# Kernel optimization log

Hardware: AMD Instinct MI355X
Metric: run time of the kernel (lower is better)

The kernel has to match this reference:

```python
import jax, jax.numpy as jnp
import numpy as np

THRESHOLD = 0.5
NEG_POS_RATIO = 3
ALPHA = 10.0
N_PRIORS = 8732
N_CLASSES = 21
BATCH = 128
N_OBJ = 32


def cxcy_to_xy(cxcy):
    return jnp.concatenate([cxcy[..., :2] - cxcy[..., 2:] / 2.0,
                            cxcy[..., :2] + cxcy[..., 2:] / 2.0], axis=-1)


def xy_to_cxcy(xy):
    return jnp.concatenate([(xy[..., :2] + xy[..., 2:]) / 2.0,
                            xy[..., 2:] - xy[..., :2]], axis=-1)


def cxcy_to_gcxgcy(cxcy, priors_cxcy):
    return jnp.concatenate([(cxcy[..., :2] - priors_cxcy[..., :2]) / (priors_cxcy[..., 2:] / 10.0),
                            jnp.log(cxcy[..., 2:] / priors_cxcy[..., 2:]) * 5.0], axis=-1)


def find_jaccard_overlap(a, b):
    # a: (M,4) xyxy, b: (P,4) xyxy -> (M,P)
    lt = jnp.maximum(a[:, None, :2], b[None, :, :2])
    rb = jnp.minimum(a[:, None, 2:], b[None, :, 2:])
    wh = jnp.clip(rb - lt, 0.0)
    inter = wh[..., 0] * wh[..., 1]
    area_a = (a[:, 2] - a[:, 0]) * (a[:, 3] - a[:, 1])
    area_b = (b[:, 2] - b[:, 0]) * (b[:, 3] - b[:, 1])
    return inter / (area_a[:, None] + area_b[None, :] - inter)


def _match_one(boxes, labels, priors_xy, priors_cxcy):
    # boxes: (M,4) xyxy, labels: (M,)
    iou = find_jaccard_overlap(boxes, priors_xy)           # (M,P)
    obj_idx = jnp.argmax(iou, axis=1)                      # best prior per object
    iou = iou.at[jnp.arange(boxes.shape[0]), obj_idx].set(1.0)
    positive = (iou >= THRESHOLD).any(axis=0)              # (P,)
    max_prior_idx = jnp.argmax(iou, axis=0)                # best object per prior
    true_cls = labels[max_prior_idx] * positive.astype(labels.dtype)
    matched = boxes[max_prior_idx]                         # (P,4)
    true_locs = cxcy_to_gcxgcy(xy_to_cxcy(matched), priors_cxcy)
    return true_locs, true_cls, positive


def setup_inputs() -> dict:
    key = jax.random.key(0)
    k1, k2, k3, k4, k5, k6 = jax.random.split(key, 6)
    pred_loc = jax.random.normal(k1, (BATCH, N_PRIORS, 4), dtype=jnp.float32)
    pred_cls = jax.random.normal(k2, (BATCH, N_PRIORS, N_CLASSES), dtype=jnp.float32)
    # valid xyxy gt boxes in [0,1]
    p1 = jax.random.uniform(k3, (BATCH, N_OBJ, 2))
    p2 = jax.random.uniform(k4, (BATCH, N_OBJ, 2))
    b_boxes = jnp.concatenate([jnp.minimum(p1, p2), jnp.maximum(p1, p2) + 1e-3], axis=-1)
    b_boxes = jnp.clip(b_boxes, 0.0, 1.0).astype(jnp.float32)
    b_labels = jax.random.randint(k5, (BATCH, N_OBJ), 1, N_CLASSES)
    cxy = jax.random.uniform(k6, (N_PRIORS, 2), minval=0.1, maxval=0.9)
    wh = jax.random.uniform(jax.random.fold_in(k6, 1), (N_PRIORS, 2), minval=0.05, maxval=0.3)
    priors_cxcy = jnp.concatenate([cxy, wh], axis=-1).astype(jnp.float32)
    return {"pred_loc": pred_loc, "pred_cls": pred_cls, "b_boxes": b_boxes,
            "b_labels": b_labels, "priors_cxcy": priors_cxcy}


def reference(pred_loc, pred_cls, b_boxes, b_labels, priors_cxcy):
    batch_size, n_priors, n_classes = pred_cls.shape
    priors_xy = cxcy_to_xy(priors_cxcy)
    true_locs, true_classes, positive = jax.vmap(
        _match_one, in_axes=(0, 0, None, None))(b_boxes, b_labels, priors_xy, priors_cxcy)
    pos_f = positive.astype(pred_loc.dtype)                 # (B,P)
    n_positives = positive.sum(axis=1)                      # (B,)
    n_pos_total = n_positives.sum().astype(pred_loc.dtype)
    # L1 loss (mean over positive box elements)
    loc_loss = (jnp.abs(pred_loc - true_locs) * pos_f[..., None]).sum() / (n_pos_total * 4.0)
    # per-prior cross-entropy
    logp = jax.nn.log_softmax(pred_cls, axis=-1)
    ce = -jnp.take_along_axis(logp, true_classes[..., None], axis=-1)[..., 0]  # (B,P)
    conf_loss_pos = (ce * pos_f).sum()
    # hard negative mining: sort negatives descending per image
    conf_neg = jnp.where(positive, 0.0, ce)
    conf_neg_sorted = -jnp.sort(-conf_neg, axis=1)
    ranks = jnp.arange(n_priors)[None, :]
    hard_mask = ranks < (NEG_POS_RATIO * n_positives)[:, None]
    conf_loss_hard_neg = jnp.where(hard_mask, conf_neg_sorted, 0.0).sum()
    conf_loss = (conf_loss_hard_neg + conf_loss_pos) / n_pos_total
    loc_loss = ALPHA * loc_loss
    total_loss = conf_loss + loc_loss
    return total_loss, loc_loss, conf_loss
```

## Files before the change

kernel.cpp:

```cpp
#include <hip/hip_runtime.h>
#include <math.h>

#define B 128
#define M 32
#define P 8732
#define C 21
#define ALPHA 10.0f
#define TPB2 256
#define PPT 4
#define PPB (TPB2 * PPT)
#define NB2 9

__global__ __launch_bounds__(256) void k1_objargmax(
    const float* __restrict__ b_boxes, const float* __restrict__ priors,
    int* __restrict__ objidx, int* __restrict__ done) {
  if (blockIdx.x == 0 && threadIdx.x == 0) *done = 0;
  int wid = threadIdx.x >> 6;
  int lane = threadIdx.x & 63;
  int task = blockIdx.x * 4 + wid;
  if (task >= B * M) return;
  const float* bx = b_boxes + (size_t)task * 4;
  float x1 = bx[0], y1 = bx[1], x2 = bx[2], y2 = bx[3];
  float areaA = (x2 - x1) * (y2 - y1);
  float best = -1.0f;
  int bi = P;
  for (int p = lane; p < P; p += 64) {
    float4 pr = ((const float4*)priors)[p];
    float pw2 = pr.z * 0.5f, ph2 = pr.w * 0.5f;
    float iw = fminf(x2, pr.x + pw2) - fmaxf(x1, pr.x - pw2);
    float ih = fminf(y2, pr.y + ph2) - fmaxf(y1, pr.y - ph2);
    iw = fmaxf(iw, 0.0f);
    ih = fmaxf(ih, 0.0f);
    float inter = iw * ih;
    float iou = inter / (areaA + pr.z * pr.w - inter);
    if (iou > best) { best = iou; bi = p; }
  }
  for (int off = 32; off >= 1; off >>= 1) {
    float ov = __shfl_xor(best, off, 64);
    int oi = __shfl_xor(bi, off, 64);
    if (ov > best || (ov == best && oi < bi)) { best = ov; bi = oi; }
  }
  if (lane == 0) objidx[task] = bi;
}

__global__ __launch_bounds__(TPB2) void k2_perprior(
    const float* __restrict__ pred_loc, const float* __restrict__ pred_cls,
    const float* __restrict__ b_boxes, const int* __restrict__ b_labels,
    const float* __restrict__ priors, const int* __restrict__ objidx,
    float* __restrict__ ploc, float* __restrict__ pce, int* __restrict__ pnp,
    float* __restrict__ confneg) {
  int b = blockIdx.y;
  int p0 = blockIdx.x * PPB;
  int tid = threadIdx.x;

  __shared__ float sx1[M], sy1[M], sx2[M], sy2[M], sarea[M];
  __shared__ int slab[M], sobj[M];
  if (tid < M) {
    int m = tid;
    float4 bx = ((const float4*)b_boxes)[b * M + m];
    sx1[m] = bx.x; sy1[m] = bx.y; sx2[m] = bx.z; sy2[m] = bx.w;
    sarea[m] = (bx.z - bx.x) * (bx.w - bx.y);
    slab[m] = b_labels[b * M + m];
    sobj[m] = objidx[b * M + m];
  }
  __syncthreads();

  float locpart = 0.0f, cepospart = 0.0f;
  int npos = 0;
  int pbase = p0 + tid * PPT;
  if (pbase < P) {
    float4 pr[PPT], pl[PPT];
    const float4* prp = (const float4*)priors + pbase;
    const float4* plp = (const float4*)pred_loc + (size_t)b * P + pbase;
#pragma unroll
    for (int j = 0; j < PPT; j++) { pr[j] = prp[j]; pl[j] = plp[j]; }

    float px1[PPT], py1[PPT], px2[PPT], py2[PPT], areaP[PPT], best[PPT];
    int bm[PPT];
#pragma unroll
    for (int j = 0; j < PPT; j++) {
      float pw2 = pr[j].z * 0.5f, ph2 = pr[j].w * 0.5f;
      px1[j] = pr[j].x - pw2; py1[j] = pr[j].y - ph2;
      px2[j] = pr[j].x + pw2; py2[j] = pr[j].y + ph2;
      areaP[j] = pr[j].z * pr[j].w;
      best[j] = -1.0f; bm[j] = 0;
    }
    for (int m = 0; m < M; m++) {
      float bx1 = sx1[m], by1 = sy1[m], bx2 = sx2[m], by2 = sy2[m];
      float ar = sarea[m];
      int so = sobj[m];
#pragma unroll
      for (int j = 0; j < PPT; j++) {
        float iw = fminf(bx2, px2[j]) - fmaxf(bx1, px1[j]);
        float ih = fminf(by2, py2[j]) - fmaxf(by1, py1[j]);
        iw = fmaxf(iw, 0.0f);
        ih = fmaxf(ih, 0.0f);
        float inter = iw * ih;
        float iou = inter / (ar + areaP[j] - inter);
        if (so == pbase + j) iou = 1.0f;
        if (iou > best[j]) { best[j] = iou; bm[j] = m; }
      }
    }

    const float4* pc4t =
        (const float4*)(pred_cls + ((size_t)b * P + p0) * C) + 21 * tid;
    float4 cn;
    float* cnp = (float*)&cn;
#pragma unroll
    for (int j = 0; j < PPT; j++) {
      bool pos = best[j] >= 0.5f;
      int mj = bm[j];
      int cls = pos ? slab[mj] : 0;
      float bx1 = sx1[mj], by1 = sy1[mj], bx2 = sx2[mj], by2 = sy2[mj];
      float cx = (bx1 + bx2) * 0.5f, cy = (by1 + by2) * 0.5f;
      float w = bx2 - bx1, h = by2 - by1;
      float g0 = (cx - pr[j].x) * 10.0f / pr[j].z;
      float g1 = (cy - pr[j].y) * 10.0f / pr[j].w;
      float g2 = __logf(w / pr[j].z) * 5.0f;
      float g3 = __logf(h / pr[j].w) * 5.0f;
      if (pos) {
        locpart += fabsf(pl[j].x - g0) + fabsf(pl[j].y - g1) +
                   fabsf(pl[j].z - g2) + fabsf(pl[j].w - g3);
        npos++;
      }
      float4 u4[6];
#pragma unroll
      for (int q = 0; q < 6; q++) u4[q] = pc4t[5 * j + q];
      const float* u = (const float*)u4;
      float mx = u[j];
#pragma unroll
      for (int c = 1; c < C; c++) mx = fmaxf(mx, u[j + c]);
      float se = 0.0f;
      float vc = u[j];
#pragma unroll
      for (int c = 0; c < C; c++) {
        float x = u[j + c];
        se += __expf(x - mx);
        if (c == cls) vc = x;
      }
      float ce = mx + __logf(se) - vc;
      cnp[j] = pos ? 0.0f : ce;
      cepospart += pos ? ce : 0.0f;
    }
    ((float4*)confneg)[((size_t)b * P + pbase) >> 2] = cn;
  }

  for (int off = 32; off >= 1; off >>= 1) {
    locpart += __shfl_down(locpart, off, 64);
    cepospart += __shfl_down(cepospart, off, 64);
    npos += __shfl_down(npos, off, 64);
  }
  __shared__ float rloc[4], rce[4];
  __shared__ int rnp[4];
  int wid = tid >> 6;
  if ((tid & 63) == 0) { rloc[wid] = locpart; rce[wid] = cepospart; rnp[wid] = npos; }
  __syncthreads();
  if (tid == 0) {
    int f = b * NB2 + blockIdx.x;
    ploc[f] = rloc[0] + rloc[1] + rloc[2] + rloc[3];
    pce[f] = rce[0] + rce[1] + rce[2] + rce[3];
    pnp[f] = rnp[0] + rnp[1] + rnp[2] + rnp[3];
  }
}

__global__ __launch_bounds__(1024) void k3_hardneg(
    const float* __restrict__ confneg,
    const float* __restrict__ ploc, const float* __restrict__ pce,
    const int* __restrict__ pnp,
    float* __restrict__ imgres, int* __restrict__ done,
    float* __restrict__ out) {
  int b = blockIdx.x;
  int tid = threadIdx.x;
  int wid = tid >> 6;
  int lane = tid & 63;

  __shared__ float s[P];
  __shared__ int histw[16 * 256];
  __shared__ __align__(16) int cnt[256];
  __shared__ int sdig, scum, sK, sLast;
  __shared__ float sLoc, sCe, sNp;
  __shared__ float rsum[16], rl[16], rc[16], rh[16], rn[16];
  __shared__ int rcnt[16];

  const float* row = confneg + (size_t)b * P;
  for (int i = tid; i < P; i += 1024) s[i] = row[i];

  if (wid == 0) {
    float lp = 0.0f, cp = 0.0f;
    int np = 0;
    if (lane < NB2) {
      int f = b * NB2 + lane;
      lp = ploc[f]; cp = pce[f]; np = pnp[f];
    }
    for (int off = 32; off >= 1; off >>= 1) {
      lp += __shfl_down(lp, off, 64);
      cp += __shfl_down(cp, off, 64);
      np += __shfl_down(np, off, 64);
    }
    if (lane == 0) {
      int K = np * 3;
      if (K > P) K = P;
      sK = K; sLoc = lp; sCe = cp; sNp = (float)np;
    }
  }
  __syncthreads();

  int K = sK;
  unsigned pfx = 0;
  int Krem = K;
#pragma unroll
  for (int pass = 3; pass >= 0; --pass) {
    int sh = pass * 8;
    for (int i = tid; i < 16 * 256; i += 1024) histw[i] = 0;
    __syncthreads();
    unsigned himask = (pass == 3) ? 0u : (0xFFFFFFFFu << (sh + 8));
    int* myh = &histw[wid * 256];
    for (int i = tid; i < P; i += 1024) {
      unsigned ub = __float_as_uint(s[i]);
      if ((ub & himask) == pfx) atomicAdd(&myh[(ub >> sh) & 255], 1);
    }
    __syncthreads();
    if (tid < 256) {
      int c = 0;
#pragma unroll
      for (int w = 0; w < 16; w++) c += histw[w * 256 + tid];
      cnt[tid] = c;
    }
    __syncthreads();
    if (wid == 0) {
      int4 c4 = ((const int4*)cnt)[lane];
      int s3 = c4.w;
      int s2 = c4.z + s3;
      int s1 = c4.y + s2;
      int s0 = c4.x + s1;
      int suf = s0;
      for (int off = 1; off < 64; off <<= 1) {
        int t = __shfl_down(suf, off, 64);
        if (lane + off < 64) suf += t;
      }
      int above = suf - s0;
      int S0 = above + s0, S1 = above + s1, S2 = above + s2, S3 = above + s3;
      int S4 = above;
      if (S3 >= Krem && S4 < Krem) { sdig = 4 * lane + 3; scum = S4; }
      else if (S2 >= Krem && S3 < Krem) { sdig = 4 * lane + 2; scum = S3; }
      else if (S1 >= Krem && S2 < Krem) { sdig = 4 * lane + 1; scum = S2; }
      else if (S0 >= Krem && S1 < Krem) { sdig = 4 * lane + 0; scum = S1; }
    }
    __syncthreads();
    pfx |= ((unsigned)sdig) << sh;
    Krem -= scum;
  }
  float tau = __uint_as_float(pfx);

  float sum = 0.0f;
  int cgt = 0;
  for (int i = tid; i < P; i += 1024) {
    float v = s[i];
    if (v > tau) { sum += v; cgt++; }
  }
  for (int off = 32; off >= 1; off >>= 1) {
    sum += __shfl_down(sum, off, 64);
    cgt += __shfl_down(cgt, off, 64);
  }
  if (lane == 0) { rsum[wid] = sum; rcnt[wid] = cgt; }
  __syncthreads();
  if (tid == 0) {
    float stot = 0.0f;
    int ctot = 0;
#pragma unroll
    for (int w = 0; w < 16; w++) { stot += rsum[w]; ctot += rcnt[w]; }
    float hard = stot + (float)(K - ctot) * tau;
    imgres[b * 4 + 0] = sLoc;
    imgres[b * 4 + 1] = sCe;
    imgres[b * 4 + 2] = hard;
    imgres[b * 4 + 3] = sNp;
    __threadfence();
    int prev = atomicAdd(done, 1);
    sLast = (prev == B - 1) ? 1 : 0;
  }
  __syncthreads();
  if (sLast) {
    __threadfence();
    float l = 0.0f, c = 0.0f, h = 0.0f, n = 0.0f;
    if (tid < B) {
      l = atomicAdd(&imgres[tid * 4 + 0], 0.0f);
      c = atomicAdd(&imgres[tid * 4 + 1], 0.0f);
      h = atomicAdd(&imgres[tid * 4 + 2], 0.0f);
      n = atomicAdd(&imgres[tid * 4 + 3], 0.0f);
    }
    for (int off = 32; off >= 1; off >>= 1) {
      l += __shfl_down(l, off, 64);
      c += __shfl_down(c, off, 64);
      h += __shfl_down(h, off, 64);
      n += __shfl_down(n, off, 64);
    }
    if (lane == 0) { rl[wid] = l; rc[wid] = c; rh[wid] = h; rn[wid] = n; }
    __syncthreads();
    if (tid == 0) {
      float L = 0, Cc = 0, H = 0, N = 0;
#pragma unroll
      for (int w = 0; w < 16; w++) { L += rl[w]; Cc += rc[w]; H += rh[w]; N += rn[w]; }
      float loc = ALPHA * L / (N * 4.0f);
      float conf = (H + Cc) / N;
      out[0] = conf + loc;
      out[1] = loc;
      out[2] = conf;
    }
  }
}

extern "C" void kernel_launch(void* const* d_in, const int* in_sizes, int n_in,
                              void* d_out, int out_size, void* d_ws, size_t ws_size,
                              hipStream_t stream) {
  (void)in_sizes; (void)n_in; (void)out_size; (void)ws_size;
  const float* pred_loc = (const float*)d_in[0];
  const float* pred_cls = (const float*)d_in[1];
  const float* b_boxes = (const float*)d_in[2];
  const int* b_labels = (const int*)d_in[3];
  const float* priors = (const float*)d_in[4];
  float* out = (float*)d_out;

  int* done = (int*)d_ws;
  float* ploc = (float*)d_ws + 8;
  float* pce = ploc + B * NB2;
  int* pnp = (int*)(pce + B * NB2);
  float* imgres = (float*)(pnp + B * NB2);
  int* objidx = (int*)(imgres + B * 4);
  float* confneg = (float*)(objidx + B * M);

  k1_objargmax<<<(B * M + 3) / 4, 256, 0, stream>>>(b_boxes, priors, objidx, done);
  dim3 g2(NB2, B);
  k2_perprior<<<g2, TPB2, 0, stream>>>(pred_loc, pred_cls, b_boxes, b_labels,
                                       priors, objidx, ploc, pce, pnp, confneg);
  k3_hardneg<<<B, 1024, 0, stream>>>(confneg, ploc, pce, pnp, imgres, done, out);
}
```

Baseline: 259.4 us.

## Divide-free IoU argmax via cross-multiplication, 4 objects per wave in k1, vectorized smem load

```diff
diff --git a/kernel.cpp b/kernel.cpp
--- a/kernel.cpp
+++ b/kernel.cpp
@@ -17,30 +17,52 @@
   if (blockIdx.x == 0 && threadIdx.x == 0) *done = 0;
   int wid = threadIdx.x >> 6;
   int lane = threadIdx.x & 63;
-  int task = blockIdx.x * 4 + wid;
-  if (task >= B * M) return;
-  const float* bx = b_boxes + (size_t)task * 4;
-  float x1 = bx[0], y1 = bx[1], x2 = bx[2], y2 = bx[3];
-  float areaA = (x2 - x1) * (y2 - y1);
-  float best = -1.0f;
-  int bi = P;
+  int b = blockIdx.x >> 1;
+  int obase = ((blockIdx.x & 1) * 4 + wid) * 4;
+
+  float ox1[4], oy1[4], ox2[4], oy2[4], oarea[4];
+  float bI[4], bU[4];
+  int bidx[4];
+#pragma unroll
+  for (int k = 0; k < 4; k++) {
+    float4 bx = ((const float4*)b_boxes)[(size_t)b * M + obase + k];
+    ox1[k] = bx.x; oy1[k] = bx.y; ox2[k] = bx.z; oy2[k] = bx.w;
+    oarea[k] = (bx.z - bx.x) * (bx.w - bx.y);
+    bI[k] = -1.0f; bU[k] = 1.0f; bidx[k] = P;
+  }
+
+#pragma unroll 4
   for (int p = lane; p < P; p += 64) {
     float4 pr = ((const float4*)priors)[p];
     float pw2 = pr.z * 0.5f, ph2 = pr.w * 0.5f;
-    float iw = fminf(x2, pr.x + pw2) - fmaxf(x1, pr.x - pw2);
-    float ih = fminf(y2, pr.y + ph2) - fmaxf(y1, pr.y - ph2);
-    iw = fmaxf(iw, 0.0f);
-    ih = fmaxf(ih, 0.0f);
-    float inter = iw * ih;
-    float iou = inter / (areaA + pr.z * pr.w - inter);
-    if (iou > best) { best = iou; bi = p; }
+    float px1 = pr.x - pw2, py1 = pr.y - ph2;
+    float px2 = pr.x + pw2, py2 = pr.y + ph2;
+    float areaP = pr.z * pr.w;
+#pragma unroll
+    for (int k = 0; k < 4; k++) {
+      float iw = fminf(ox2[k], px2) - fmaxf(ox1[k], px1);
+      float ih = fminf(oy2[k], py2) - fmaxf(oy1[k], py1);
+      iw = fmaxf(iw, 0.0f);
+      ih = fmaxf(ih, 0.0f);
+      float inter = iw * ih;
+      float uni = oarea[k] + areaP - inter;
+      if (inter * bU[k] > bI[k] * uni) { bI[k] = inter; bU[k] = uni; bidx[k] = p; }
+    }
   }
   for (int off = 32; off >= 1; off >>= 1) {
-    float ov = __shfl_xor(best, off, 64);
-    int oi = __shfl_xor(bi, off, 64);
-    if (ov > best || (ov == best && oi < bi)) { best = ov; bi = oi; }
-  }
-  if (lane == 0) objidx[task] = bi;
+#pragma unroll
+    for (int k = 0; k < 4; k++) {
+      float oI = __shfl_xor(bI[k], off, 64);
+      float oU = __shfl_xor(bU[k], off, 64);
+      int oi = __shfl_xor(bidx[k], off, 64);
+      float l = oI * bU[k], r = bI[k] * oU;
+      if (l > r || (l == r && oi < bidx[k])) { bI[k] = oI; bU[k] = oU; bidx[k] = oi; }
+    }
+  }
+  if (lane == 0) {
+#pragma unroll
+    for (int k = 0; k < 4; k++) objidx[(size_t)b * M + obase + k] = bidx[k];
+  }
 }
 
 __global__ __launch_bounds__(TPB2) void k2_perprior(
@@ -75,7 +97,8 @@
 #pragma unroll
     for (int j = 0; j < PPT; j++) { pr[j] = prp[j]; pl[j] = plp[j]; }
 
-    float px1[PPT], py1[PPT], px2[PPT], py2[PPT], areaP[PPT], best[PPT];
+    float px1[PPT], py1[PPT], px2[PPT], py2[PPT], areaP[PPT];
+    float bI[PPT], bU[PPT];
     int bm[PPT];
 #pragma unroll
     for (int j = 0; j < PPT; j++) {
@@ -83,7 +106,7 @@
       px1[j] = pr[j].x - pw2; py1[j] = pr[j].y - ph2;
       px2[j] = pr[j].x + pw2; py2[j] = pr[j].y + ph2;
       areaP[j] = pr[j].z * pr[j].w;
-      best[j] = -1.0f; bm[j] = 0;
+      bI[j] = -1.0f; bU[j] = 1.0f; bm[j] = 0;
     }
     for (int m = 0; m < M; m++) {
       float bx1 = sx1[m], by1 = sy1[m], bx2 = sx2[m], by2 = sy2[m];
@@ -96,9 +119,9 @@
         iw = fmaxf(iw, 0.0f);
         ih = fmaxf(ih, 0.0f);
         float inter = iw * ih;
-        float iou = inter / (ar + areaP[j] - inter);
-        if (so == pbase + j) iou = 1.0f;
-        if (iou > best[j]) { best[j] = iou; bm[j] = m; }
+        float uni = ar + areaP[j] - inter;
+        if (so == pbase + j) { inter = 1.0f; uni = 1.0f; }
+        if (inter * bU[j] > bI[j] * uni) { bI[j] = inter; bU[j] = uni; bm[j] = m; }
       }
     }
 
@@ -108,7 +131,7 @@
     float* cnp = (float*)&cn;
 #pragma unroll
     for (int j = 0; j < PPT; j++) {
-      bool pos = best[j] >= 0.5f;
+      bool pos = (2.0f * bI[j] >= bU[j]);
       int mj = bm[j];
       int cls = pos ? slab[mj] : 0;
       float bx1 = sx1[mj], by1 = sy1[mj], bx2 = sx2[mj], by2 = sy2[mj];
@@ -174,7 +197,7 @@
   int wid = tid >> 6;
   int lane = tid & 63;
 
-  __shared__ float s[P];
+  __shared__ __align__(16) float s[P];
   __shared__ int histw[16 * 256];
   __shared__ __align__(16) int cnt[256];
   __shared__ int sdig, scum, sK, sLast;
@@ -182,8 +205,10 @@
   __shared__ float rsum[16], rl[16], rc[16], rh[16], rn[16];
   __shared__ int rcnt[16];
 
-  const float* row = confneg + (size_t)b * P;
-  for (int i = tid; i < P; i += 1024) s[i] = row[i];
+  {
+    const float4* row4 = (const float4*)(confneg + (size_t)b * P);
+    for (int i = tid; i < P / 4; i += 1024) ((float4*)s)[i] = row4[i];
+  }
 
   if (wid == 0) {
     float lp = 0.0f, cp = 0.0f;
@@ -328,7 +353,7 @@
   int* objidx = (int*)(imgres + B * 4);
   float* confneg = (float*)(objidx + B * M);
 
-  k1_objargmax<<<(B * M + 3) / 4, 256, 0, stream>>>(b_boxes, priors, objidx, done);
+  k1_objargmax<<<B * 2, 256, 0, stream>>>(b_boxes, priors, objidx, done);
   dim3 g2(NB2, B);
   k2_perprior<<<g2, TPB2, 0, stream>>>(pred_loc, pred_cls, b_boxes, b_labels,
                                        priors, objidx, ploc, pce, pnp, confneg);
```

Result: faster. 239.0 us (-7.9%).
